# Optimization experiments

Hardware: AMD Instinct MI355X
Metric: run time of the kernel (lower is better)

The kernel has to match this reference:

```python
import jax, jax.numpy as jnp
import numpy as np

N_NODES = 100000
N_EDGES = 625000
D_IN = 128
D_OUT = 128
N_ETYPES = 64


def setup_inputs() -> dict:
    key = jax.random.key(0)
    k1, k2, k3, k4, k5, k6 = jax.random.split(key, 6)
    node_features = jax.random.normal(k1, (N_NODES, D_IN), dtype=jnp.float32)
    edge_index = jax.random.randint(k2, (2, N_EDGES), 0, N_NODES, dtype=jnp.int64)
    edge_type = jax.random.randint(k3, (N_EDGES,), 0, N_ETYPES, dtype=jnp.int64)
    edge_emb = jax.random.normal(k4, (N_ETYPES, D_OUT), dtype=jnp.float32)
    W = jax.random.normal(k5, (D_IN, D_OUT), dtype=jnp.float32) / np.sqrt(D_IN)
    b = jax.random.normal(k6, (D_OUT,), dtype=jnp.float32) * 0.01
    return {"node_features": node_features, "edge_index": edge_index,
            "edge_type": edge_type, "edge_emb": edge_emb, "W": W, "b": b}


def reference(node_features, edge_index, edge_type, edge_emb, W, b):
    # Linear transform of node features: (N, D_out)
    h = node_features @ W + b
    src, tgt = edge_index[0], edge_index[1]
    # Per-edge message: gather src feature + edge-type embedding  (E, D_out)
    messages = h[src] + edge_emb[edge_type]
    # Scatter-add into target nodes
    aggregated = jax.ops.segment_sum(messages, tgt, num_segments=N_NODES)
    # Self contribution + ReLU
    return jax.nn.relu(aggregated + h)
```

## Files before the change

### kernel.cpp

```cpp
#include <hip/hip_runtime.h>
#include <hip/hip_bf16.h>

#define D 128

typedef __attribute__((ext_vector_type(8))) short short8v;
typedef __attribute__((ext_vector_type(4))) float float4v;

__device__ __forceinline__ unsigned short f2bf(float f) {
  union { float f; unsigned int u; } v; v.f = f;
  unsigned int r = v.u + 0x7fffu + ((v.u >> 16) & 1u);
  return (unsigned short)(r >> 16);
}
__device__ __forceinline__ unsigned int pkbf(float lo, float hi) {
  float2 f; f.x = lo; f.y = hi;
  __hip_bfloat162 v = __float22bfloat162_rn(f);
  union { __hip_bfloat162 b; unsigned int u; } c; c.b = v;
  return c.u;
}
__device__ __forceinline__ float bflo(unsigned int u) {
  union { unsigned int v; float f; } c; c.v = u << 16; return c.f;
}
__device__ __forceinline__ float bfhi(unsigned int u) {
  union { unsigned int v; float f; } c; c.v = u & 0xffff0000u; return c.f;
}

__global__ __launch_bounds__(256) void prep_kernel(
    const float* __restrict__ W, const float* __restrict__ eemb,
    unsigned short* __restrict__ Wt, unsigned short* __restrict__ em_bf,
    unsigned short* __restrict__ h_bf, int* __restrict__ counts,
    int n_nodes) {
  int i = blockIdx.x * 256 + threadIdx.x;
  if (i < D * D) Wt[i] = f2bf(W[(i & 127) * D + (i >> 7)]);
  if (i < 64 * D) em_bf[i] = f2bf(eemb[i]);
  if (i < 64) ((unsigned int*)(h_bf + (size_t)n_nodes * D))[i] = 0u;
  if (i >= 64 && i < 128) ((unsigned int*)(em_bf + 64 * D))[i - 64] = 0u;
  if (i < n_nodes) counts[i] = 0;
}

__global__ __launch_bounds__(256) void gemm_h_kernel(
    const float* __restrict__ nf, const unsigned short* __restrict__ Wt,
    const float* __restrict__ b, unsigned short* __restrict__ h_bf,
    const int* __restrict__ eidx_tgt, int* __restrict__ counts,
    int n_nodes, int n_edges, int epb) {
  __shared__ float Xs[64 * D];
  const int tid = threadIdx.x;
  const int wv = tid >> 6;
  const int ln = tid & 63;
  const int nodeBase = blockIdx.x * 64;

  const char* nf_tile = (const char*)(nf + (size_t)nodeBase * D);
  char* xs_b = (char*)Xs;

  if (nodeBase + 64 <= n_nodes) {
    #pragma unroll
    for (int it = 0; it < 8; ++it) {
      const int doff = wv * 8192 + it * 1024;
      const int off = doff + ln * 16;
      const int src = off ^ (((off >> 9) & 7) << 4);
      __builtin_amdgcn_global_load_lds(
          (const __attribute__((address_space(1))) unsigned int*)(nf_tile + src),
          (__attribute__((address_space(3))) unsigned int*)(xs_b + doff),
          16, 0, 0);
    }
  } else {
    #pragma unroll
    for (int it = 0; it < 8; ++it) {
      const int off = (it * 256 + tid) * 16;
      const int src = off ^ (((off >> 9) & 7) << 4);
      const int row = src >> 9;
      float4 v = {0.f, 0.f, 0.f, 0.f};
      if (nodeBase + row < n_nodes) v = *(const float4*)(nf_tile + src);
      *(float4*)(xs_b + off) = v;
    }
  }

  {
    const int ebase = blockIdx.x * epb;
    int eend = ebase + epb;
    if (eend > n_edges) eend = n_edges;
    for (int e = ebase + tid; e < eend; e += 256)
      atomicAdd(&counts[eidx_tgt[e]], 1);
  }

  const int m = ln & 15;
  const int q = ln >> 4;
  const int n0 = (wv & 1) * 64;
  const int nodeHalf = (wv >> 1) * 32;

  short8v afrag[4][4];
  #pragma unroll
  for (int nt = 0; nt < 4; ++nt) {
    const int n = n0 + nt * 16 + m;
    #pragma unroll
    for (int kc = 0; kc < 4; ++kc)
      afrag[nt][kc] = *(const short8v*)&Wt[n * D + kc * 32 + q * 8];
  }

  float4v acc[4][2] = {};
  __syncthreads();

  #pragma unroll
  for (int kc = 0; kc < 4; ++kc) {
    #pragma unroll
    for (int t = 0; t < 2; ++t) {
      const int node = nodeHalf + t * 16 + m;
      const int ba = node * 512 + kc * 128 + q * 32;
      const int sw = (node & 7) << 4;
      const float4 x0 = *(const float4*)(xs_b + (ba ^ sw));
      const float4 x1 = *(const float4*)(xs_b + ((ba + 16) ^ sw));
      union { unsigned int u[4]; short8v s; } cv;
      cv.u[0] = pkbf(x0.x, x0.y);
      cv.u[1] = pkbf(x0.z, x0.w);
      cv.u[2] = pkbf(x1.x, x1.y);
      cv.u[3] = pkbf(x1.z, x1.w);
      const short8v bv = cv.s;
      #pragma unroll
      for (int nt = 0; nt < 4; ++nt)
        acc[nt][t] = __builtin_amdgcn_mfma_f32_16x16x32_bf16(
            afrag[nt][kc], bv, acc[nt][t], 0, 0, 0);
    }
  }

  #pragma unroll
  for (int nt = 0; nt < 4; ++nt) {
    const int colBase = n0 + nt * 16 + q * 4;
    const float4 bv = *(const float4*)&b[colBase];
    #pragma unroll
    for (int t = 0; t < 2; ++t) {
      const int node = nodeBase + nodeHalf + t * 16 + m;
      if (node < n_nodes) {
        uint2 val;
        val.x = pkbf(acc[nt][t][0] + bv.x, acc[nt][t][1] + bv.y);
        val.y = pkbf(acc[nt][t][2] + bv.z, acc[nt][t][3] + bv.w);
        *(uint2*)&h_bf[(size_t)node * D + colBase] = val;
      }
    }
  }
}

__global__ __launch_bounds__(256) void scan1_kernel(
    const int* __restrict__ counts, int* __restrict__ offsets,
    int* __restrict__ blockSums, int n) {
  __shared__ int lds[256];
  const int tid = threadIdx.x;
  const int base = blockIdx.x * 1024 + tid * 4;
  int v[4];
  #pragma unroll
  for (int k = 0; k < 4; ++k) v[k] = (base + k < n) ? counts[base + k] : 0;
  int s = v[0] + v[1] + v[2] + v[3];
  lds[tid] = s;
  for (int off = 1; off < 256; off <<= 1) {
    __syncthreads();
    int t = (tid >= off) ? lds[tid - off] : 0;
    __syncthreads();
    lds[tid] += t;
  }
  __syncthreads();
  int run = lds[tid] - s;
  #pragma unroll
  for (int k = 0; k < 4; ++k) {
    if (base + k < n) offsets[base + k] = run;
    run += v[k];
  }
  if (tid == 255) blockSums[blockIdx.x] = lds[255];
}

__global__ __launch_bounds__(256) void scan23_kernel(
    int* __restrict__ offsets, int* __restrict__ cursor,
    const int* __restrict__ blockSums, int nb, int n, int n_edges) {
  __shared__ int lds[256];
  const int tid = threadIdx.x;
  const int bid = blockIdx.x;
  lds[tid] = (tid < bid && tid < nb) ? blockSums[tid] : 0;
  __syncthreads();
  #pragma unroll
  for (int off = 128; off > 0; off >>= 1) {
    if (tid < off) lds[tid] += lds[tid + off];
    __syncthreads();
  }
  const int add = lds[0];
  const int base = bid * 1024 + tid * 4;
  #pragma unroll
  for (int k = 0; k < 4; ++k) {
    int i = base + k;
    if (i < n) {
      int o = offsets[i] + add;
      offsets[i] = o;
      cursor[i] = o;
    }
  }
  if (bid == 0 && tid == 0) offsets[n] = n_edges;
}

__global__ __launch_bounds__(256) void scatter_kernel(
    const int* __restrict__ eidx, const int* __restrict__ etype,
    int* __restrict__ cursor, unsigned int* __restrict__ packed, int n_edges) {
  const int e0 = (blockIdx.x * 256 + threadIdx.x) * 4;
  if (e0 + 3 < n_edges) {
    const int4 s4 = *(const int4*)&eidx[e0];
    const int4 t4 = *(const int4*)&eidx[n_edges + e0];
    const int4 y4 = *(const int4*)&etype[e0];
    int pos;
    pos = atomicAdd(&cursor[t4.x], 1);
    packed[pos] = (unsigned int)s4.x | ((unsigned int)y4.x << 17);
    pos = atomicAdd(&cursor[t4.y], 1);
    packed[pos] = (unsigned int)s4.y | ((unsigned int)y4.y << 17);
    pos = atomicAdd(&cursor[t4.z], 1);
    packed[pos] = (unsigned int)s4.z | ((unsigned int)y4.z << 17);
    pos = atomicAdd(&cursor[t4.w], 1);
    packed[pos] = (unsigned int)s4.w | ((unsigned int)y4.w << 17);
  } else {
    for (int e = e0; e < n_edges; ++e) {
      const int pos = atomicAdd(&cursor[eidx[n_edges + e]], 1);
      packed[pos] = (unsigned int)eidx[e] | ((unsigned int)etype[e] << 17);
    }
  }
}

__global__ __launch_bounds__(256) void aggregate_kernel(
    const int* __restrict__ offsets, const unsigned int* __restrict__ packed,
    const uint2* __restrict__ e4, const uint2* __restrict__ h4,
    float* __restrict__ out, int n_nodes, int n_edges, unsigned int zero_p) {
  const int gid = blockIdx.x * 256 + threadIdx.x;
  const int lane = threadIdx.x & 63;
  const int half = lane >> 5;
  const int sl = lane & 31;
  const int n = (gid >> 6) * 2 + half;
  if (n >= n_nodes) return;

  const uint2 sb = h4[(size_t)n * 32 + sl];
  float a0 = bflo(sb.x), a1 = bfhi(sb.x), a2 = bflo(sb.y), a3 = bfhi(sb.y);
  float c0 = 0.f, c1 = 0.f, c2 = 0.f, c3 = 0.f;

  int j = offsets[n];
  const int end = offsets[n + 1];
  int trips = (end - j + 7) >> 3;
  int to = __shfl_xor(trips, 32);
  const int T = trips > to ? trips : to;
  const int emax = n_edges - 1;

  for (int t = 0; t < T; ++t, j += 8) {
    unsigned int p[8];
    #pragma unroll
    for (int u = 0; u < 8; ++u) {
      const int ju = j + u;
      const unsigned int pu = packed[ju <= emax ? ju : emax];
      p[u] = (ju < end) ? pu : zero_p;
    }
    uint2 g[8], ev[8];
    #pragma unroll
    for (int u = 0; u < 8; ++u)
      g[u] = h4[(size_t)(p[u] & 0x1FFFFu) * 32 + sl];
    #pragma unroll
    for (int u = 0; u < 8; ++u)
      ev[u] = e4[(p[u] >> 17) * 32 + sl];
    #pragma unroll
    for (int u = 0; u < 8; u += 2) {
      a0 += bflo(g[u].x) + bflo(ev[u].x);
      a1 += bfhi(g[u].x) + bfhi(ev[u].x);
      a2 += bflo(g[u].y) + bflo(ev[u].y);
      a3 += bfhi(g[u].y) + bfhi(ev[u].y);
      c0 += bflo(g[u + 1].x) + bflo(ev[u + 1].x);
      c1 += bfhi(g[u + 1].x) + bfhi(ev[u + 1].x);
      c2 += bflo(g[u + 1].y) + bflo(ev[u + 1].y);
      c3 += bfhi(g[u + 1].y) + bfhi(ev[u + 1].y);
    }
  }

  float4 r;
  r.x = fmaxf(a0 + c0, 0.f);
  r.y = fmaxf(a1 + c1, 0.f);
  r.z = fmaxf(a2 + c2, 0.f);
  r.w = fmaxf(a3 + c3, 0.f);
  ((float4*)out)[(size_t)n * 32 + sl] = r;
}

extern "C" void kernel_launch(void* const* d_in, const int* in_sizes, int n_in,
                              void* d_out, int out_size, void* d_ws,
                              size_t ws_size, hipStream_t stream) {
  const float* nf   = (const float*)d_in[0];
  const int*   eidx = (const int*)d_in[1];
  const int*   etyp = (const int*)d_in[2];
  const float* eemb = (const float*)d_in[3];
  const float* W    = (const float*)d_in[4];
  const float* b    = (const float*)d_in[5];

  const int n_nodes = in_sizes[0] / D;
  const int n_edges = in_sizes[2];

  float* out = (float*)d_out;

  char* base = (char*)d_ws;
  unsigned short* Wt = (unsigned short*)base;
  unsigned short* em_bf = (unsigned short*)(base + 32768);
  unsigned short* h_bf = (unsigned short*)(base + 65536);
  char* tail = base + 65536 + (size_t)(n_nodes + 1) * D * 2;
  int* counts = (int*)tail;
  int* offsets = counts + n_nodes;
  int* cursor = offsets + (n_nodes + 1);
  int* blockSums = cursor + n_nodes;
  unsigned int* packed = (unsigned int*)(blockSums + 1024);

  const int nb = (n_nodes + 1023) / 1024;
  const int gemmBlocks = (n_nodes + 63) / 64;
  const int epb = (n_edges + gemmBlocks - 1) / gemmBlocks;

  prep_kernel<<<(n_nodes + 255) / 256, 256, 0, stream>>>(W, eemb, Wt, em_bf,
                                                         h_bf, counts, n_nodes);

  gemm_h_kernel<<<gemmBlocks, 256, 0, stream>>>(
      nf, Wt, b, h_bf, eidx + n_edges, counts, n_nodes, n_edges, epb);

  scan1_kernel<<<nb, 256, 0, stream>>>(counts, offsets, blockSums, n_nodes);
  scan23_kernel<<<nb, 256, 0, stream>>>(offsets, cursor, blockSums, nb,
                                        n_nodes, n_edges);

  scatter_kernel<<<(n_edges + 1023) / 1024, 256, 0, stream>>>(
      eidx, etyp, cursor, packed, n_edges);

  const unsigned int zero_p = (unsigned int)n_nodes | (64u << 17);
  const int aggBlocks = (n_nodes + 7) / 8;
  aggregate_kernel<<<aggBlocks, 256, 0, stream>>>(
      offsets, packed, (const uint2*)em_bf, (const uint2*)h_bf, out, n_nodes,
      n_edges, zero_p);
}
```

Baseline: 131.0 us.

## Drop LDS staging in node GEMM and shrink aggregate unroll to four

The node-transform GEMM no longer stages a 64x128 fp32 tile in LDS. Each wave now loads its 16 node rows straight from global memory into bf16 B fragments and streams the W fragments per output tile, covering all 128 columns. This removes the LDS allocation and the block barrier, and moves the edge-count atomics after the GEMM. The aggregate kernel processes 4 edges per iteration instead of 8, which lowers register pressure and padding waste for low-degree nodes but leaves fewer gathers in flight per iteration.

After: 141.6 us. 1.08x slower.

```diff
diff --git a/kernel.cpp b/kernel.cpp
--- a/kernel.cpp
+++ b/kernel.cpp
@@ -42,100 +42,59 @@
     const float* __restrict__ b, unsigned short* __restrict__ h_bf,
     const int* __restrict__ eidx_tgt, int* __restrict__ counts,
     int n_nodes, int n_edges, int epb) {
-  __shared__ float Xs[64 * D];
   const int tid = threadIdx.x;
   const int wv = tid >> 6;
   const int ln = tid & 63;
-  const int nodeBase = blockIdx.x * 64;
-
-  const char* nf_tile = (const char*)(nf + (size_t)nodeBase * D);
-  char* xs_b = (char*)Xs;
-
-  if (nodeBase + 64 <= n_nodes) {
-    #pragma unroll
-    for (int it = 0; it < 8; ++it) {
-      const int doff = wv * 8192 + it * 1024;
-      const int off = doff + ln * 16;
-      const int src = off ^ (((off >> 9) & 7) << 4);
-      __builtin_amdgcn_global_load_lds(
-          (const __attribute__((address_space(1))) unsigned int*)(nf_tile + src),
-          (__attribute__((address_space(3))) unsigned int*)(xs_b + doff),
-          16, 0, 0);
-    }
-  } else {
-    #pragma unroll
-    for (int it = 0; it < 8; ++it) {
-      const int off = (it * 256 + tid) * 16;
-      const int src = off ^ (((off >> 9) & 7) << 4);
-      const int row = src >> 9;
-      float4 v = {0.f, 0.f, 0.f, 0.f};
-      if (nodeBase + row < n_nodes) v = *(const float4*)(nf_tile + src);
-      *(float4*)(xs_b + off) = v;
-    }
-  }
-
-  {
-    const int ebase = blockIdx.x * epb;
-    int eend = ebase + epb;
-    if (eend > n_edges) eend = n_edges;
-    for (int e = ebase + tid; e < eend; e += 256)
-      atomicAdd(&counts[eidx_tgt[e]], 1);
-  }
-
   const int m = ln & 15;
   const int q = ln >> 4;
-  const int n0 = (wv & 1) * 64;
-  const int nodeHalf = (wv >> 1) * 32;
-
-  short8v afrag[4][4];
-  #pragma unroll
-  for (int nt = 0; nt < 4; ++nt) {
-    const int n = n0 + nt * 16 + m;
+  const int node = blockIdx.x * 64 + wv * 16 + m;
+  const int row = node < n_nodes ? node : n_nodes - 1;
+  const float* xrow = nf + (size_t)row * D;
+
+  short8v bfrag[4];
+  #pragma unroll
+  for (int kc = 0; kc < 4; ++kc) {
+    const float4 x0 = *(const float4*)(xrow + kc * 32 + q * 8);
+    const float4 x1 = *(const float4*)(xrow + kc * 32 + q * 8 + 4);
+    union { unsigned int u[4]; short8v s; } cv;
+    cv.u[0] = pkbf(x0.x, x0.y);
+    cv.u[1] = pkbf(x0.z, x0.w);
+    cv.u[2] = pkbf(x1.x, x1.y);
+    cv.u[3] = pkbf(x1.z, x1.w);
+    bfrag[kc] = cv.s;
+  }
+
+  float4v acc[8] = {};
+  #pragma unroll
+  for (int nt = 0; nt < 8; ++nt) {
+    const unsigned short* wrow = Wt + (nt * 16 + m) * D + q * 8;
+    const short8v a0 = *(const short8v*)(wrow);
+    const short8v a1 = *(const short8v*)(wrow + 32);
+    const short8v a2 = *(const short8v*)(wrow + 64);
+    const short8v a3 = *(const short8v*)(wrow + 96);
+    acc[nt] = __builtin_amdgcn_mfma_f32_16x16x32_bf16(a0, bfrag[0], acc[nt], 0, 0, 0);
+    acc[nt] = __builtin_amdgcn_mfma_f32_16x16x32_bf16(a1, bfrag[1], acc[nt], 0, 0, 0);
+    acc[nt] = __builtin_amdgcn_mfma_f32_16x16x32_bf16(a2, bfrag[2], acc[nt], 0, 0, 0);
+    acc[nt] = __builtin_amdgcn_mfma_f32_16x16x32_bf16(a3, bfrag[3], acc[nt], 0, 0, 0);
+  }
+
+  if (node < n_nodes) {
+    unsigned short* orow = h_bf + (size_t)node * D + q * 4;
     #pragma unroll
-    for (int kc = 0; kc < 4; ++kc)
-      afrag[nt][kc] = *(const short8v*)&Wt[n * D + kc * 32 + q * 8];
-  }
-
-  float4v acc[4][2] = {};
-  __syncthreads();
-
-  #pragma unroll
-  for (int kc = 0; kc < 4; ++kc) {
-    #pragma unroll
-    for (int t = 0; t < 2; ++t) {
-      const int node = nodeHalf + t * 16 + m;
-      const int ba = node * 512 + kc * 128 + q * 32;
-      const int sw = (node & 7) << 4;
-      const float4 x0 = *(const float4*)(xs_b + (ba ^ sw));
-      const float4 x1 = *(const float4*)(xs_b + ((ba + 16) ^ sw));
-      union { unsigned int u[4]; short8v s; } cv;
-      cv.u[0] = pkbf(x0.x, x0.y);
-      cv.u[1] = pkbf(x0.z, x0.w);
-      cv.u[2] = pkbf(x1.x, x1.y);
-      cv.u[3] = pkbf(x1.z, x1.w);
-      const short8v bv = cv.s;
-      #pragma unroll
-      for (int nt = 0; nt < 4; ++nt)
-        acc[nt][t] = __builtin_amdgcn_mfma_f32_16x16x32_bf16(
-            afrag[nt][kc], bv, acc[nt][t], 0, 0, 0);
+    for (int nt = 0; nt < 8; ++nt) {
+      const float4 bv = *(const float4*)&b[nt * 16 + q * 4];
+      uint2 val;
+      val.x = pkbf(acc[nt][0] + bv.x, acc[nt][1] + bv.y);
+      val.y = pkbf(acc[nt][2] + bv.z, acc[nt][3] + bv.w);
+      *(uint2*)(orow + nt * 16) = val;
     }
   }
 
-  #pragma unroll
-  for (int nt = 0; nt < 4; ++nt) {
-    const int colBase = n0 + nt * 16 + q * 4;
-    const float4 bv = *(const float4*)&b[colBase];
-    #pragma unroll
-    for (int t = 0; t < 2; ++t) {
-      const int node = nodeBase + nodeHalf + t * 16 + m;
-      if (node < n_nodes) {
-        uint2 val;
-        val.x = pkbf(acc[nt][t][0] + bv.x, acc[nt][t][1] + bv.y);
-        val.y = pkbf(acc[nt][t][2] + bv.z, acc[nt][t][3] + bv.w);
-        *(uint2*)&h_bf[(size_t)node * D + colBase] = val;
-      }
-    }
-  }
+  const int ebase = blockIdx.x * epb;
+  int eend = ebase + epb;
+  if (eend > n_edges) eend = n_edges;
+  for (int e = ebase + tid; e < eend; e += 256)
+    atomicAdd(&counts[eidx_tgt[e]], 1);
 }
 
 __global__ __launch_bounds__(256) void scan1_kernel(
@@ -234,37 +193,37 @@
 
   int j = offsets[n];
   const int end = offsets[n + 1];
-  int trips = (end - j + 7) >> 3;
+  int trips = (end - j + 3) >> 2;
   int to = __shfl_xor(trips, 32);
   const int T = trips > to ? trips : to;
   const int emax = n_edges - 1;
 
-  for (int t = 0; t < T; ++t, j += 8) {
-    unsigned int p[8];
-    #pragma unroll
-    for (int u = 0; u < 8; ++u) {
-      const int ju = j + u;
-      const unsigned int pu = packed[ju <= emax ? ju : emax];
-      p[u] = (ju < end) ? pu : zero_p;
-    }
-    uint2 g[8], ev[8];
-    #pragma unroll
-    for (int u = 0; u < 8; ++u)
-      g[u] = h4[(size_t)(p[u] & 0x1FFFFu) * 32 + sl];
-    #pragma unroll
-    for (int u = 0; u < 8; ++u)
-      ev[u] = e4[(p[u] >> 17) * 32 + sl];
-    #pragma unroll
-    for (int u = 0; u < 8; u += 2) {
-      a0 += bflo(g[u].x) + bflo(ev[u].x);
-      a1 += bfhi(g[u].x) + bfhi(ev[u].x);
-      a2 += bflo(g[u].y) + bflo(ev[u].y);
-      a3 += bfhi(g[u].y) + bfhi(ev[u].y);
-      c0 += bflo(g[u + 1].x) + bflo(ev[u + 1].x);
-      c1 += bfhi(g[u + 1].x) + bfhi(ev[u + 1].x);
-      c2 += bflo(g[u + 1].y) + bflo(ev[u + 1].y);
-      c3 += bfhi(g[u + 1].y) + bfhi(ev[u + 1].y);
-    }
+  for (int t = 0; t < T; ++t, j += 4) {
+    const int j1 = j + 1, j2 = j + 2, j3 = j + 3;
+    unsigned int p0 = packed[j  <= emax ? j  : emax];
+    unsigned int p1 = packed[j1 <= emax ? j1 : emax];
+    unsigned int p2 = packed[j2 <= emax ? j2 : emax];
+    unsigned int p3 = packed[j3 <= emax ? j3 : emax];
+    p0 = (j  < end) ? p0 : zero_p;
+    p1 = (j1 < end) ? p1 : zero_p;
+    p2 = (j2 < end) ? p2 : zero_p;
+    p3 = (j3 < end) ? p3 : zero_p;
+    const uint2 g0 = h4[(size_t)(p0 & 0x1FFFFu) * 32 + sl];
+    const uint2 g1 = h4[(size_t)(p1 & 0x1FFFFu) * 32 + sl];
+    const uint2 g2 = h4[(size_t)(p2 & 0x1FFFFu) * 32 + sl];
+    const uint2 g3 = h4[(size_t)(p3 & 0x1FFFFu) * 32 + sl];
+    const uint2 e0 = e4[(p0 >> 17) * 32 + sl];
+    const uint2 e1 = e4[(p1 >> 17) * 32 + sl];
+    const uint2 e2 = e4[(p2 >> 17) * 32 + sl];
+    const uint2 e3 = e4[(p3 >> 17) * 32 + sl];
+    a0 += bflo(g0.x) + bflo(e0.x); a1 += bfhi(g0.x) + bfhi(e0.x);
+    a2 += bflo(g0.y) + bflo(e0.y); a3 += bfhi(g0.y) + bfhi(e0.y);
+    c0 += bflo(g1.x) + bflo(e1.x); c1 += bfhi(g1.x) + bfhi(e1.x);
+    c2 += bflo(g1.y) + bflo(e1.y); c3 += bfhi(g1.y) + bfhi(e1.y);
+    a0 += bflo(g2.x) + bflo(e2.x); a1 += bfhi(g2.x) + bfhi(e2.x);
+    a2 += bflo(g2.y) + bflo(e2.y); a3 += bfhi(g2.y) + bfhi(e2.y);
+    c0 += bflo(g3.x) + bflo(e3.x); c1 += bfhi(g3.x) + bfhi(e3.x);
+    c2 += bflo(g3.y) + bflo(e3.y); c3 += bfhi(g3.y) + bfhi(e3.y);
   }
 
   float4 r;
```
